# Kernel tuning notes

Measured on AMD Instinct MI355X. Metric: run time of the kernel, lower is better.

## Reference

```python
import jax, jax.numpy as jnp
import numpy as np

B, S, D = 8, 1024, 1152
H, HD = 16, 72  # num_heads, head_dim

def setup_inputs() -> dict:
    key = jax.random.key(0)
    ks = jax.random.split(key, 7)
    hidden_states = jax.random.normal(ks[0], (B, S, D), dtype=jnp.float32)
    cos = jax.random.uniform(ks[1], (S, HD), dtype=jnp.float32)
    sin = jax.random.uniform(ks[2], (S, HD), dtype=jnp.float32)
    qkv_w = jax.random.normal(ks[3], (3 * D, D), dtype=jnp.float32) * 0.02
    qkv_b = jnp.zeros((3 * D,), dtype=jnp.float32)
    proj_w = jax.random.normal(ks[4], (D, D), dtype=jnp.float32) * 0.02
    proj_b = jnp.zeros((D,), dtype=jnp.float32)
    return {"hidden_states": hidden_states, "cos": cos, "sin": sin,
            "qkv_w": qkv_w, "qkv_b": qkv_b, "proj_w": proj_w, "proj_b": proj_b}

def _rotate_half(x):
    x1, x2 = jnp.split(x, 2, axis=-1)
    return jnp.concatenate((-x2, x1), axis=-1)

def reference(hidden_states, cos, sin, qkv_w, qkv_b, proj_w, proj_b):
    b, s, d = hidden_states.shape
    # fused QKV projection
    qkv = hidden_states @ qkv_w.T + qkv_b            # [B,S,3D]
    qkv = qkv.reshape(b, s, 3, H, HD)
    qkv = jnp.transpose(qkv, (2, 0, 3, 1, 4))        # [3,B,H,S,HD]
    q, k, v = qkv[0], qkv[1], qkv[2]
    # rotary embedding, cos/sin broadcast [1,1,S,HD]
    c = cos[None, None, :, :]
    sn = sin[None, None, :, :]
    q = q * c + _rotate_half(q) * sn
    k = k * c + _rotate_half(k) * sn
    # SDPA
    scale = HD ** -0.5
    scores = jnp.einsum('bhqd,bhkd->bhqk', q, k) * scale
    probs = jax.nn.softmax(scores, axis=-1)
    attn = jnp.einsum('bhqk,bhkd->bhqd', probs, v)   # [B,H,S,HD]
    attn = jnp.transpose(attn, (0, 2, 1, 3)).reshape(b, s, d)
    return attn @ proj_w.T + proj_b
```

## Files before the change

kernel.cpp:

```cpp
#include <hip/hip_runtime.h>
#include <hip/hip_bf16.h>


typedef __attribute__((ext_vector_type(8))) short short8;
typedef __attribute__((ext_vector_type(4))) float f32x4;

__device__ __forceinline__ unsigned int f2bf(float f) {
    unsigned int u = __float_as_uint(f);
    return (u + 0x7FFFu + ((u >> 16) & 1u)) >> 16;
}
__device__ __forceinline__ float bf2f(unsigned short u) {
    return __uint_as_float((unsigned int)u << 16);
}

__device__ __forceinline__ unsigned int pk_bf16(float a, float b) {
    unsigned int r;
    asm("v_cvt_pk_bf16_f32 %0, %1, %2" : "=v"(r) : "v"(a), "v"(b));
    return r;
}

__device__ __forceinline__ void stout(float* C, size_t idx, float v) { C[idx] = v; }
__device__ __forceinline__ void stout(__hip_bfloat16* C, size_t idx, float v) {
    C[idx] = __float2bfloat16(v);
}

__device__ __forceinline__ void async_cp16(const void* g, void* l) {
    __builtin_amdgcn_global_load_lds((const __attribute__((address_space(1))) void*)g,
                                     (__attribute__((address_space(3))) void*)l, 16, 0, 0);
}

__global__ void f32_to_bf16_pair(
    const float* __restrict__ s0, unsigned short* __restrict__ d0, int n0_4,
    const float* __restrict__ s1, unsigned short* __restrict__ d1, int n1_4,
    unsigned short* __restrict__ dz, int nz_4)
{
    int i = blockIdx.x * 256 + threadIdx.x;
    if (i < n0_4) {
        float4 f = ((const float4*)s0)[i];
        ushort4 r;
        r.x = (unsigned short)f2bf(f.x);
        r.y = (unsigned short)f2bf(f.y);
        r.z = (unsigned short)f2bf(f.z);
        r.w = (unsigned short)f2bf(f.w);
        ((ushort4*)d0)[i] = r;
        return;
    }
    i -= n0_4;
    if (i < n1_4) {
        float4 f = ((const float4*)s1)[i];
        ushort4 r;
        r.x = (unsigned short)f2bf(f.x);
        r.y = (unsigned short)f2bf(f.y);
        r.z = (unsigned short)f2bf(f.z);
        r.w = (unsigned short)f2bf(f.w);
        ((ushort4*)d1)[i] = r;
        return;
    }
    i -= n1_4;
    if (i < nz_4) {
        ushort4 z; z.x = 0; z.y = 0; z.z = 0; z.w = 0;
        ((ushort4*)dz)[i] = z;
    }
}

template <int BM, int H>
__device__ __forceinline__ void stage_a(const unsigned short* __restrict__ g, int ldg,
                                        int k0, unsigned short* l, int w, int lane)
{
    if constexpr (BM == 256) {
#pragma unroll
        for (int t = 0; t < 2; t++) {
            const int c  = w * 2 + t;
            const int r0 = (c & 8) * 16 + H * 64 + (c & 7) * 8;
            const int rl = r0 + (lane >> 3);
            const int gg = (lane & 7) ^ (lane >> 3);
            async_cp16(g + (size_t)rl * ldg + k0 + gg * 8, l + r0 * 64);
        }
    } else {
        const int c  = w;
        const int r0 = (c & 4) * 16 + H * 32 + (c & 3) * 8;
        const int rl = r0 + (lane >> 3);
        const int gg = (lane & 7) ^ (lane >> 3);
        async_cp16(g + (size_t)rl * ldg + k0 + gg * 8, l + r0 * 64);
    }
}

template <int H>
__device__ __forceinline__ void stage_b(const unsigned short* __restrict__ g, int ldg,
                                        int k0, unsigned short* l, int w, int lane)
{
#pragma unroll
    for (int t = 0; t < 2; t++) {
        const int c  = w * 2 + t;
        const int r0 = (c >> 2) * 64 + H * 32 + (c & 3) * 8;
        const int rl = r0 + (lane >> 3);
        const int gg = (lane & 7) ^ (lane >> 3);
        async_cp16(g + (size_t)rl * ldg + k0 + gg * 8, l + r0 * 64);
    }
}

#define LDA(MH, SRC)                                                                   \
    _Pragma("unroll") for (int mi = 0; mi < MFRAG_; ++mi) {                            \
        Af[mi][0] = *(const short8*)((SRC) + aRow + (MH) * (BM * 16) + mi * 1024 + g0); \
        Af[mi][1] = *(const short8*)((SRC) + aRow + (MH) * (BM * 16) + mi * 1024 + g1); \
    }

#define LDB(DST, NH, SRC)                                                         \
    _Pragma("unroll") for (int ni = 0; ni < 2; ++ni) {                            \
        DST[ni][0] = *(const short8*)((SRC) + bRow + (NH) * 2048 + ni * 1024 + g0); \
        DST[ni][1] = *(const short8*)((SRC) + bRow + (NH) * 2048 + ni * 1024 + g1); \
    }

#define MFMAS(MH, NH, PB)                                                              \
    __builtin_amdgcn_s_setprio(1);                                                     \
    _Pragma("unroll") for (int mi = 0; mi < MFRAG_; ++mi)                              \
    _Pragma("unroll") for (int ni = 0; ni < 2; ++ni) {                                 \
        acc[(MH) * MFRAG_ + mi][(NH) * 2 + ni] = __builtin_amdgcn_mfma_f32_16x16x32_bf16( \
            Af[mi][0], PB[ni][0], acc[(MH) * MFRAG_ + mi][(NH) * 2 + ni], 0, 0, 0);    \
        acc[(MH) * MFRAG_ + mi][(NH) * 2 + ni] = __builtin_amdgcn_mfma_f32_16x16x32_bf16( \
            Af[mi][1], PB[ni][1], acc[(MH) * MFRAG_ + mi][(NH) * 2 + ni], 0, 0, 0);    \
    }                                                                                  \
    __builtin_amdgcn_s_setprio(0);

#define MIDBAR()                                                   \
    do {                                                           \
        __builtin_amdgcn_s_barrier();                              \
        asm volatile("s_waitcnt lgkmcnt(0)" ::: "memory");         \
        __builtin_amdgcn_sched_barrier(0);                         \
    } while (0)

#define ENDBAR()                                                   \
    do {                                                           \
        __builtin_amdgcn_s_barrier();                              \
        __builtin_amdgcn_sched_barrier(0);                         \
    } while (0)

#define GVMCNT()                                                          \
    do {                                                                  \
        if constexpr (BM == 256)                                          \
            asm volatile("s_waitcnt vmcnt(6)" ::: "memory");              \
        else                                                              \
            asm volatile("s_waitcnt vmcnt(4)" ::: "memory");              \
    } while (0)

template <typename OT, int BM>
__global__ __launch_bounds__(512, 2) void gemm_bt_256(
    const __hip_bfloat16* __restrict__ Abf,
    const __hip_bfloat16* __restrict__ Bbf,
    const float* __restrict__ bias,
    OT* __restrict__ C,
    int M, int Nreal, int K)
{
    constexpr int MFRAG_ = BM / 64;
    __shared__ __align__(16) unsigned short smem[2][(BM + 256) * 64];

    const int tid  = threadIdx.x;
    const int lane = tid & 63;
    const int w    = tid >> 6;
    const int wm   = w >> 2;
    const int wn   = w & 3;
    const int q    = lane >> 4;
    const int fr   = lane & 15;
    const int xr   = fr & 7;

    const int nwg = gridDim.x * gridDim.y;
    const int lin = blockIdx.y * gridDim.x + blockIdx.x;
    const int swz = (lin & 7) * (nwg >> 3) + (lin >> 3);
    const int bn  = (swz % gridDim.x) * 256;
    const int bm  = (swz / gridDim.x) * BM;

    const unsigned short* Ag = (const unsigned short*)Abf + (size_t)bm * K;
    const unsigned short* Bg = (const unsigned short*)Bbf + (size_t)bn * K;

    unsigned short* s00 = &smem[0][0];
    unsigned short* s01 = &smem[0][BM * 64];
    unsigned short* s10 = &smem[1][0];
    unsigned short* s11 = &smem[1][BM * 64];

    const int NT = K >> 6;
    const int NI = NT >> 1;

    const int aRow = (wm * (BM / 2) + fr) * 64;
    const int bRow = (wn * 64 + fr) * 64;
    const int g0   = ((0 * 4 + q) ^ xr) * 8;
    const int g1   = ((1 * 4 + q) ^ xr) * 8;

    f32x4 acc[2 * MFRAG_][4];
#pragma unroll
    for (int i = 0; i < 2 * MFRAG_; i++)
#pragma unroll
        for (int j = 0; j < 4; j++) acc[i][j] = (f32x4){0.f, 0.f, 0.f, 0.f};

    short8 Af[MFRAG_][2], Bf0[2][2], Bf1[2][2];

    stage_a<BM, 0>(Ag, K, 0, s00, w, lane);
    stage_a<BM, 1>(Ag, K, 0, s00, w, lane);
    stage_b<0>(Bg, K, 0, s01, w, lane);
    stage_b<1>(Bg, K, 0, s01, w, lane);
    stage_a<BM, 0>(Ag, K, 64, s10, w, lane);
    stage_b<1>(Bg, K, 64, s11, w, lane);
    stage_a<BM, 1>(Ag, K, 64, s10, w, lane);
    GVMCNT();
    ENDBAR();

#pragma unroll 1
    for (int i = 0; i < NI; i++) {
        const int k1 = (2 * i + 1) * 64;
        const int t2 = 2 * i + 2, t3 = 2 * i + 3;
        const int k2 = (t2 < NT ? t2 : NT - 1) * 64;
        const int k3 = (t3 < NT ? t3 : NT - 1) * 64;

        LDA(0, s00);
        LDB(Bf0, 0, s01);
        stage_b<0>(Bg, K, k1, s11, w, lane);
        asm volatile("s_waitcnt lgkmcnt(8)" ::: "memory");
        MIDBAR();
        MFMAS(0, 0, Bf0);
        ENDBAR();

        LDB(Bf1, 1, s01);
        stage_a<BM, 0>(Ag, K, k2, s00, w, lane);
        MIDBAR();
        MFMAS(0, 1, Bf1);
        ENDBAR();

        LDA(1, s00);
        stage_b<1>(Bg, K, k2, s01, w, lane);
        MIDBAR();
        MFMAS(1, 1, Bf1);
        ENDBAR();

        stage_a<BM, 1>(Ag, K, k2, s00, w, lane);
        GVMCNT();
        MIDBAR();
        MFMAS(1, 0, Bf0);
        ENDBAR();

        LDA(0, s10);
        LDB(Bf0, 0, s11);
        stage_b<0>(Bg, K, k2, s01, w, lane);
        asm volatile("s_waitcnt lgkmcnt(8)" ::: "memory");
        MIDBAR();
        MFMAS(0, 0, Bf0);
        ENDBAR();

        LDB(Bf1, 1, s11);
        stage_a<BM, 0>(Ag, K, k3, s10, w, lane);
        MIDBAR();
        MFMAS(0, 1, Bf1);
        ENDBAR();

        LDA(1, s10);
        stage_b<1>(Bg, K, k3, s11, w, lane);
        MIDBAR();
        MFMAS(1, 1, Bf1);
        ENDBAR();

        stage_a<BM, 1>(Ag, K, k3, s10, w, lane);
        GVMCNT();
        MIDBAR();
        MFMAS(1, 0, Bf0);
        ENDBAR();
    }

#pragma unroll
    for (int mf = 0; mf < 2 * MFRAG_; mf++) {
        const int row = bm + wm * (BM / 2) + mf * 16 + q * 4;
#pragma unroll
        for (int nf = 0; nf < 4; nf++) {
            const int col = bn + wn * 64 + nf * 16 + fr;
            if (col < Nreal) {
                const float bv = bias[col];
#pragma unroll
                for (int r = 0; r < 4; r++)
                    stout(C, (size_t)(row + r) * Nreal + col, acc[mf][nf][r] + bv);
            }
        }
    }
}

__global__ void rope_v_prep(
    const __hip_bfloat16* __restrict__ qkv,
    const float* __restrict__ cosp,
    const float* __restrict__ sinp,
    __hip_bfloat16* __restrict__ Qo,
    __hip_bfloat16* __restrict__ Ko,
    __hip_bfloat16* __restrict__ Vt)
{
    __shared__ __align__(16) unsigned short T[64 * 72];
    const int tid = threadIdx.x;
    const int bh = blockIdx.x >> 4;
    const int st = blockIdx.x & 15;
    const int b = bh >> 4, h = bh & 15;
    const size_t row0 = ((size_t)b * 1024 + st * 64) * 3456;

    const unsigned short* vsrc = (const unsigned short*)qkv + row0 + 2304 + h * 72;
#pragma unroll
    for (int k = 0; k < 3; k++) {
        const int c = tid + k * 256;
        if (c < 576) {
            const int s = c / 9, off = (c % 9) * 8;
            *(uint4*)&T[c * 8] = *(const uint4*)(vsrc + (size_t)s * 3456 + off);
        }
    }

    const unsigned short* qkvp = (const unsigned short*)qkv;
    const float QS = 0.17002324f;
#pragma unroll
    for (int k = 0; k < 3; k++) {
        const int idx = tid + k * 256;
        if (idx < 576) {
            const int sl = idx / 9, iq = idx % 9;
            const int i0 = iq * 4;
            const int sg = st * 64 + sl;
            const unsigned short* qrow = qkvp + row0 + (size_t)sl * 3456 + h * 72 + i0;

            ushort4 ql = *(const ushort4*)(qrow);
            ushort4 qh = *(const ushort4*)(qrow + 36);
            ushort4 kl = *(const ushort4*)(qrow + 1152);
            ushort4 kh = *(const ushort4*)(qrow + 1188);
            float4 cl = *(const float4*)(cosp + sg * 72 + i0);
            float4 ch = *(const float4*)(cosp + sg * 72 + i0 + 36);
            float4 nl = *(const float4*)(sinp + sg * 72 + i0);
            float4 nh = *(const float4*)(sinp + sg * 72 + i0 + 36);

            unsigned short qlv[4] = {ql.x, ql.y, ql.z, ql.w};
            unsigned short qhv[4] = {qh.x, qh.y, qh.z, qh.w};
            unsigned short klv[4] = {kl.x, kl.y, kl.z, kl.w};
            unsigned short khv[4] = {kh.x, kh.y, kh.z, kh.w};
            float clv[4] = {cl.x, cl.y, cl.z, cl.w};
            float chv[4] = {ch.x, ch.y, ch.z, ch.w};
            float nlv[4] = {nl.x, nl.y, nl.z, nl.w};
            float nhv[4] = {nh.x, nh.y, nh.z, nh.w};

            unsigned short qol[4], qoh[4], kol[4], koh[4];
#pragma unroll
            for (int j = 0; j < 4; j++) {
                const float qa = bf2f(qlv[j]), qb = bf2f(qhv[j]);
                const float ka = bf2f(klv[j]), kb = bf2f(khv[j]);
                qol[j] = (unsigned short)f2bf((qa * clv[j] - qb * nlv[j]) * QS);
                qoh[j] = (unsigned short)f2bf((qb * chv[j] + qa * nhv[j]) * QS);
                kol[j] = (unsigned short)f2bf(ka * clv[j] - kb * nlv[j]);
                koh[j] = (unsigned short)f2bf(kb * chv[j] + ka * nhv[j]);
            }
            unsigned short* qob = (unsigned short*)Qo + ((size_t)bh * 1024 + sg) * 72 + i0;
            unsigned short* kob = (unsigned short*)Ko + ((size_t)bh * 1024 + sg) * 72 + i0;
            *(ushort4*)qob        = (ushort4){qol[0], qol[1], qol[2], qol[3]};
            *(ushort4*)(qob + 36) = (ushort4){qoh[0], qoh[1], qoh[2], qoh[3]};
            *(ushort4*)kob        = (ushort4){kol[0], kol[1], kol[2], kol[3]};
            *(ushort4*)(kob + 36) = (ushort4){koh[0], koh[1], koh[2], koh[3]};
        }
    }

    __syncthreads();

    unsigned short* dst = (unsigned short*)Vt + (size_t)(bh * 16 + st) * 72 * 64;
#pragma unroll
    for (int k = 0; k < 9; k++) {
        const int o = tid + k * 256;
        const int d = o >> 5;
        const int sl = (o & 31) * 2;
        ushort2 v;
        v.x = T[sl * 72 + d];
        v.y = T[(sl + 1) * 72 + d];
        const int col = ((((sl >> 3) ^ (d & 7)) << 3)) + (sl & 7);
        *(ushort2*)&dst[d * 64 + col] = v;
    }
}

__device__ __forceinline__ void dma9(const unsigned short* g, unsigned short* l,
                                     int w, int lane)
{
#pragma unroll
    for (int c = 0; c < 3; c++) {
        const int i = w + c * 4;
        if (i < 9) async_cp16(g + i * 512 + lane * 8, l + i * 512);
    }
}

__global__ __launch_bounds__(256, 3) void attn_mfma(
    const __hip_bfloat16* __restrict__ Q,
    const __hip_bfloat16* __restrict__ K,
    const __hip_bfloat16* __restrict__ Vt,
    __hip_bfloat16* __restrict__ O)
{
    __shared__ __align__(16) unsigned short Ks[64 * 72];
    __shared__ __align__(16) unsigned short VsA[2][72 * 64];
    __shared__ __align__(16) unsigned short Vones[8 * 64];
    __shared__ __align__(16) unsigned short Ps[4][32][72];

    const int tid  = threadIdx.x;
    const int lane = tid & 63;
    const int w    = tid >> 6;
    const int quad = lane >> 4;
    const int fr   = lane & 15;
    const int bh   = blockIdx.x & 127;
    const int qt   = blockIdx.x >> 7;
    const int qbase = qt * 128 + w * 32;

    const short8 z8 = (short8){0,0,0,0,0,0,0,0};

    for (int idx = tid; idx < 512; idx += 256)
        Vones[idx] = (idx < 64) ? (unsigned short)0x3F80 : (unsigned short)0;

    const unsigned short* qp = (const unsigned short*)Q + ((size_t)bh * 1024 + qbase + fr) * 72;
    short8 qf[2][3];
#pragma unroll
    for (int sub = 0; sub < 2; sub++) {
        const unsigned short* qs = qp + sub * 16 * 72;
        qf[sub][0] = *(const short8*)(qs + quad * 8);
        qf[sub][1] = *(const short8*)(qs + 32 + quad * 8);
        qf[sub][2] = (quad == 0) ? *(const short8*)(qs + 64) : z8;
    }

    f32x4 Oa[2][5];
#pragma unroll
    for (int sub = 0; sub < 2; sub++)
#pragma unroll
        for (int n = 0; n < 5; n++) Oa[sub][n] = (f32x4){0.f, 0.f, 0.f, 0.f};

    const unsigned short* kg0 = (const unsigned short*)K + (size_t)bh * 1024 * 72;
    const unsigned short* vg0 = (const unsigned short*)Vt + (size_t)bh * 16 * 72 * 64;

    dma9(kg0, Ks, w, lane);
    dma9(vg0, &VsA[0][0], w, lane);
    dma9(vg0 + 4608, &VsA[1][0], w, lane);
    __builtin_amdgcn_sched_barrier(0);

#pragma unroll 1
    for (int t = 0; t < 16; t++) {
        if (t < 15) {
            if (w == 0) asm volatile("s_waitcnt vmcnt(3)" ::: "memory");
            else        asm volatile("s_waitcnt vmcnt(2)" ::: "memory");
        } else {
            asm volatile("s_waitcnt vmcnt(0)" ::: "memory");
        }
        __builtin_amdgcn_sched_barrier(0);
        __builtin_amdgcn_s_barrier();

        const unsigned short* vb = &VsA[t & 1][0];

#pragma unroll
        for (int nt = 0; nt < 4; nt++) {
            const unsigned short* kr = Ks + (nt * 16 + fr) * 72;
            short8 b0 = *(const short8*)(kr + quad * 8);
            short8 b1 = *(const short8*)(kr + 32 + quad * 8);
            short8 b2 = (quad == 0) ? *(const short8*)(kr + 64) : z8;
            f32x4 s0 = (f32x4){0.f, 0.f, 0.f, 0.f};
            f32x4 s1 = (f32x4){0.f, 0.f, 0.f, 0.f};
            __builtin_amdgcn_s_setprio(1);
            s0 = __builtin_amdgcn_mfma_f32_16x16x32_bf16(b0, qf[0][0], s0, 0, 0, 0);
            s1 = __builtin_amdgcn_mfma_f32_16x16x32_bf16(b0, qf[1][0], s1, 0, 0, 0);
            s0 = __builtin_amdgcn_mfma_f32_16x16x32_bf16(b1, qf[0][1], s0, 0, 0, 0);
            s1 = __builtin_amdgcn_mfma_f32_16x16x32_bf16(b1, qf[1][1], s1, 0, 0, 0);
            s0 = __builtin_amdgcn_mfma_f32_16x16x32_bf16(b2, qf[0][2], s0, 0, 0, 0);
            s1 = __builtin_amdgcn_mfma_f32_16x16x32_bf16(b2, qf[1][2], s1, 0, 0, 0);
            __builtin_amdgcn_s_setprio(0);
            uint2 p0, p1;
            p0.x = pk_bf16(__builtin_amdgcn_exp2f(s0[0]), __builtin_amdgcn_exp2f(s0[1]));
            p0.y = pk_bf16(__builtin_amdgcn_exp2f(s0[2]), __builtin_amdgcn_exp2f(s0[3]));
            p1.x = pk_bf16(__builtin_amdgcn_exp2f(s1[0]), __builtin_amdgcn_exp2f(s1[1]));
            p1.y = pk_bf16(__builtin_amdgcn_exp2f(s1[2]), __builtin_amdgcn_exp2f(s1[3]));
            *(uint2*)&Ps[w][fr][nt * 16 + quad * 4]      = p0;
            *(uint2*)&Ps[w][16 + fr][nt * 16 + quad * 4] = p1;
        }

        __builtin_amdgcn_s_barrier();
        __builtin_amdgcn_sched_barrier(0);
        if (t < 15) {
            dma9(kg0 + (size_t)(t + 1) * 4608, Ks, w, lane);
            __builtin_amdgcn_sched_barrier(0);
        }

#pragma unroll
        for (int ks = 0; ks < 2; ks++) {
            short8 ap0 = *(const short8*)&Ps[w][fr][ks * 32 + quad * 8];
            short8 ap1 = *(const short8*)&Ps[w][16 + fr][ks * 32 + quad * 8];
            const int jx8 = ((ks * 4 + quad) ^ (fr & 7)) * 8;
#pragma unroll
            for (int n = 0; n < 5; n++) {
                const unsigned short* p =
                    (n < 4) ? (vb + (n * 16 + fr) * 64 + jx8)
                            : ((fr < 8) ? (vb + (64 + fr) * 64 + jx8)
                                        : (&Vones[0] + (fr - 8) * 64 + jx8));
                short8 bv = *(const short8*)p;
                __builtin_amdgcn_s_setprio(1);
                Oa[0][n] = __builtin_amdgcn_mfma_f32_16x16x32_bf16(ap0, bv, Oa[0][n], 0, 0, 0);
                Oa[1][n] = __builtin_amdgcn_mfma_f32_16x16x32_bf16(ap1, bv, Oa[1][n], 0, 0, 0);
                __builtin_amdgcn_s_setprio(0);
            }
        }

        __builtin_amdgcn_s_barrier();
        __builtin_amdgcn_sched_barrier(0);
        if (t < 14) {
            dma9(vg0 + (size_t)(t + 2) * 4608, &VsA[t & 1][0], w, lane);
            __builtin_amdgcn_sched_barrier(0);
        }
    }

    const int lsrc = (lane & 48) | 8;
    const int b = bh >> 4, h = bh & 15;
    unsigned short* ob = (unsigned short*)O;
#pragma unroll
    for (int sub = 0; sub < 2; sub++) {
        float inv[4];
#pragma unroll
        for (int r = 0; r < 4; r++)
            inv[r] = 1.f / __shfl(Oa[sub][4][r], lsrc, 64);
#pragma unroll
        for (int n = 0; n < 5; n++) {
            const int d = n * 16 + fr;
            if (d < 72) {
#pragma unroll
                for (int r = 0; r < 4; r++) {
                    const size_t idx =
                        ((size_t)b * 1024 + qbase + sub * 16 + quad * 4 + r) * 1152 + h * 72 + d;
                    ob[idx] = (unsigned short)f2bf(Oa[sub][n][r] * inv[r]);
                }
            }
        }
    }
}

extern "C" void kernel_launch(void* const* d_in, const int* in_sizes, int n_in,
                              void* d_out, int out_size, void* d_ws, size_t ws_size,
                              hipStream_t stream)
{
    const float* hs     = (const float*)d_in[0];
    const float* cosp   = (const float*)d_in[1];
    const float* sinp   = (const float*)d_in[2];
    const float* qkv_w  = (const float*)d_in[3];
    const float* qkv_b  = (const float*)d_in[4];
    const float* proj_w = (const float*)d_in[5];
    const float* proj_b = (const float*)d_in[6];
    float* out = (float*)d_out;

    char* ws = (char*)d_ws;
    __hip_bfloat16* qkv_buf = (__hip_bfloat16*)ws;
    __hip_bfloat16* Qb = (__hip_bfloat16*)(ws + 56623104);
    __hip_bfloat16* Kb = Qb + 9437184;
    __hip_bfloat16* Vt = Kb + 9437184;
    __hip_bfloat16* Ab = qkv_buf;

    unsigned short* hs_bf = (unsigned short*)Qb;
    unsigned short* qw_bf = (unsigned short*)Kb;
    unsigned short* pw_bf = (unsigned short*)Qb;

    f32_to_bf16_pair<<<13248, 256, 0, stream>>>(hs, hs_bf, 2359296,
                                                qkv_w, qw_bf, 995328,
                                                qw_bf + 3981312, 36864);
    gemm_bt_256<__hip_bfloat16, 256>
        <<<dim3(14, 32), 512, 0, stream>>>((const __hip_bfloat16*)hs_bf,
                                           (const __hip_bfloat16*)qw_bf,
                                           qkv_b, qkv_buf, 8192, 3456, 1152);
    rope_v_prep<<<2048, 256, 0, stream>>>(qkv_buf, cosp, sinp, Qb, Kb, Vt);
    attn_mfma<<<1024, 256, 0, stream>>>(Qb, Kb, Vt, Ab);
    f32_to_bf16_pair<<<1440, 256, 0, stream>>>(proj_w, pw_bf, 331776,
                                               nullptr, nullptr, 0,
                                               pw_bf + 1327104, 36864);
    gemm_bt_256<float, 128>
        <<<dim3(5, 64), 512, 0, stream>>>((const __hip_bfloat16*)Ab,
                                          (const __hip_bfloat16*)pw_bf,
                                          proj_b, out, 8192, 1152, 1152);
}
```

Measured before the change: 303.3 us.

## Double-buffer K tiles in attention and fold proj_w conversion into first cast kernel

The attention kernel now double-buffers K alongside V, issuing one combined K+V prefetch two tiles ahead. This removes the mid-iteration barrier and K reload that used to sit between the QK and PV phases. The extra LDS lowers launch bounds from 3 to 2 blocks per CU, which risks lower occupancy. Separately, when the workspace is large enough, proj_w is converted to bf16 in the initial cast kernel into a tail region, which removes one kernel launch.

```diff
diff --git a/kernel.cpp b/kernel.cpp
--- a/kernel.cpp
+++ b/kernel.cpp
@@ -29,38 +29,52 @@
                                      (__attribute__((address_space(3))) void*)l, 16, 0, 0);
 }
 
+__device__ __forceinline__ void cvt4(const float* __restrict__ s,
+                                     unsigned short* __restrict__ d, int i)
+{
+    float4 f = ((const float4*)s)[i];
+    ushort4 r;
+    r.x = (unsigned short)f2bf(f.x);
+    r.y = (unsigned short)f2bf(f.y);
+    r.z = (unsigned short)f2bf(f.z);
+    r.w = (unsigned short)f2bf(f.w);
+    ((ushort4*)d)[i] = r;
+}
+
 __global__ void f32_to_bf16_pair(
     const float* __restrict__ s0, unsigned short* __restrict__ d0, int n0_4,
     const float* __restrict__ s1, unsigned short* __restrict__ d1, int n1_4,
     unsigned short* __restrict__ dz, int nz_4)
 {
     int i = blockIdx.x * 256 + threadIdx.x;
-    if (i < n0_4) {
-        float4 f = ((const float4*)s0)[i];
-        ushort4 r;
-        r.x = (unsigned short)f2bf(f.x);
-        r.y = (unsigned short)f2bf(f.y);
-        r.z = (unsigned short)f2bf(f.z);
-        r.w = (unsigned short)f2bf(f.w);
-        ((ushort4*)d0)[i] = r;
-        return;
-    }
+    if (i < n0_4) { cvt4(s0, d0, i); return; }
     i -= n0_4;
-    if (i < n1_4) {
-        float4 f = ((const float4*)s1)[i];
-        ushort4 r;
-        r.x = (unsigned short)f2bf(f.x);
-        r.y = (unsigned short)f2bf(f.y);
-        r.z = (unsigned short)f2bf(f.z);
-        r.w = (unsigned short)f2bf(f.w);
-        ((ushort4*)d1)[i] = r;
-        return;
-    }
+    if (i < n1_4) { cvt4(s1, d1, i); return; }
     i -= n1_4;
     if (i < nz_4) {
         ushort4 z; z.x = 0; z.y = 0; z.z = 0; z.w = 0;
         ((ushort4*)dz)[i] = z;
     }
+}
+
+__global__ void f32_to_bf16_tri(
+    const float* __restrict__ s0, unsigned short* __restrict__ d0, int n0_4,
+    const float* __restrict__ s1, unsigned short* __restrict__ d1, int n1_4,
+    unsigned short* __restrict__ dz1, int nz1_4,
+    const float* __restrict__ s2, unsigned short* __restrict__ d2, int n2_4,
+    unsigned short* __restrict__ dz2, int nz2_4)
+{
+    int i = blockIdx.x * 256 + threadIdx.x;
+    if (i < n0_4) { cvt4(s0, d0, i); return; }
+    i -= n0_4;
+    if (i < n1_4) { cvt4(s1, d1, i); return; }
+    i -= n1_4;
+    ushort4 z; z.x = 0; z.y = 0; z.z = 0; z.w = 0;
+    if (i < nz1_4) { ((ushort4*)dz1)[i] = z; return; }
+    i -= nz1_4;
+    if (i < n2_4) { cvt4(s2, d2, i); return; }
+    i -= n2_4;
+    if (i < nz2_4) ((ushort4*)dz2)[i] = z;
 }
 
 template <int BM, int H>
@@ -368,23 +382,30 @@
     }
 }
 
-__device__ __forceinline__ void dma9(const unsigned short* g, unsigned short* l,
-                                     int w, int lane)
-{
-#pragma unroll
-    for (int c = 0; c < 3; c++) {
-        const int i = w + c * 4;
-        if (i < 9) async_cp16(g + i * 512 + lane * 8, l + i * 512);
-    }
-}
-
-__global__ __launch_bounds__(256, 3) void attn_mfma(
+__device__ __forceinline__ void attn_stage(const unsigned short* kt, const unsigned short* vt,
+                                           unsigned short* kl, unsigned short* vl,
+                                           int w, int lane)
+{
+#pragma unroll
+    for (int c = 0; c < 5; c++) {
+        const int call = w + c * 4;
+        if (call < 18) {
+            const bool isv = (call >= 9);
+            const int o = (isv ? call - 9 : call) * 512;
+            const unsigned short* s = (isv ? vt : kt) + o + lane * 8;
+            unsigned short* d = (isv ? vl : kl) + o;
+            async_cp16(s, d);
+        }
+    }
+}
+
+__global__ __launch_bounds__(256, 2) void attn_mfma(
     const __hip_bfloat16* __restrict__ Q,
     const __hip_bfloat16* __restrict__ K,
     const __hip_bfloat16* __restrict__ Vt,
     __hip_bfloat16* __restrict__ O)
 {
-    __shared__ __align__(16) unsigned short Ks[64 * 72];
+    __shared__ __align__(16) unsigned short KsA[2][64 * 72];
     __shared__ __align__(16) unsigned short VsA[2][72 * 64];
     __shared__ __align__(16) unsigned short Vones[8 * 64];
     __shared__ __align__(16) unsigned short Ps[4][32][72];
@@ -422,27 +443,27 @@
     const unsigned short* kg0 = (const unsigned short*)K + (size_t)bh * 1024 * 72;
     const unsigned short* vg0 = (const unsigned short*)Vt + (size_t)bh * 16 * 72 * 64;
 
-    dma9(kg0, Ks, w, lane);
-    dma9(vg0, &VsA[0][0], w, lane);
-    dma9(vg0 + 4608, &VsA[1][0], w, lane);
+    attn_stage(kg0,        vg0,        &KsA[0][0], &VsA[0][0], w, lane);
+    attn_stage(kg0 + 4608, vg0 + 4608, &KsA[1][0], &VsA[1][0], w, lane);
     __builtin_amdgcn_sched_barrier(0);
 
 #pragma unroll 1
     for (int t = 0; t < 16; t++) {
         if (t < 15) {
-            if (w == 0) asm volatile("s_waitcnt vmcnt(3)" ::: "memory");
-            else        asm volatile("s_waitcnt vmcnt(2)" ::: "memory");
+            if (w < 2) asm volatile("s_waitcnt vmcnt(5)" ::: "memory");
+            else       asm volatile("s_waitcnt vmcnt(4)" ::: "memory");
         } else {
             asm volatile("s_waitcnt vmcnt(0)" ::: "memory");
         }
         __builtin_amdgcn_sched_barrier(0);
         __builtin_amdgcn_s_barrier();
 
-        const unsigned short* vb = &VsA[t & 1][0];
+        const unsigned short* kb = (t & 1) ? &KsA[1][0] : &KsA[0][0];
+        const unsigned short* vb = (t & 1) ? &VsA[1][0] : &VsA[0][0];
 
 #pragma unroll
         for (int nt = 0; nt < 4; nt++) {
-            const unsigned short* kr = Ks + (nt * 16 + fr) * 72;
+            const unsigned short* kr = kb + (nt * 16 + fr) * 72;
             short8 b0 = *(const short8*)(kr + quad * 8);
             short8 b1 = *(const short8*)(kr + 32 + quad * 8);
             short8 b2 = (quad == 0) ? *(const short8*)(kr + 64) : z8;
@@ -465,13 +486,6 @@
             *(uint2*)&Ps[w][16 + fr][nt * 16 + quad * 4] = p1;
         }
 
-        __builtin_amdgcn_s_barrier();
-        __builtin_amdgcn_sched_barrier(0);
-        if (t < 15) {
-            dma9(kg0 + (size_t)(t + 1) * 4608, Ks, w, lane);
-            __builtin_amdgcn_sched_barrier(0);
-        }
-
 #pragma unroll
         for (int ks = 0; ks < 2; ks++) {
             short8 ap0 = *(const short8*)&Ps[w][fr][ks * 32 + quad * 8];
@@ -493,8 +507,12 @@
 
         __builtin_amdgcn_s_barrier();
         __builtin_amdgcn_sched_barrier(0);
+
         if (t < 14) {
-            dma9(vg0 + (size_t)(t + 2) * 4608, &VsA[t & 1][0], w, lane);
+            unsigned short* kd = (t & 1) ? &KsA[1][0] : &KsA[0][0];
+            unsigned short* vd = (t & 1) ? &VsA[1][0] : &VsA[0][0];
+            attn_stage(kg0 + (size_t)(t + 2) * 4608, vg0 + (size_t)(t + 2) * 4608,
+                       kd, vd, w, lane);
             __builtin_amdgcn_sched_barrier(0);
         }
     }
@@ -545,20 +563,32 @@
 
     unsigned short* hs_bf = (unsigned short*)Qb;
     unsigned short* qw_bf = (unsigned short*)Kb;
-    unsigned short* pw_bf = (unsigned short*)Qb;
-
-    f32_to_bf16_pair<<<13248, 256, 0, stream>>>(hs, hs_bf, 2359296,
-                                                qkv_w, qw_bf, 995328,
-                                                qw_bf + 3981312, 36864);
+
+    const bool tail_ok = (ws_size >= (size_t)113246208 + 2949120);
+    unsigned short* pw_bf = tail_ok ? (unsigned short*)(ws + 113246208)
+                                    : (unsigned short*)Qb;
+
+    if (tail_ok) {
+        f32_to_bf16_tri<<<14688, 256, 0, stream>>>(
+            hs, hs_bf, 2359296,
+            qkv_w, qw_bf, 995328, qw_bf + 3981312, 36864,
+            proj_w, pw_bf, 331776, pw_bf + 1327104, 36864);
+    } else {
+        f32_to_bf16_pair<<<13248, 256, 0, stream>>>(hs, hs_bf, 2359296,
+                                                    qkv_w, qw_bf, 995328,
+                                                    qw_bf + 3981312, 36864);
+    }
     gemm_bt_256<__hip_bfloat16, 256>
         <<<dim3(14, 32), 512, 0, stream>>>((const __hip_bfloat16*)hs_bf,
                                            (const __hip_bfloat16*)qw_bf,
                                            qkv_b, qkv_buf, 8192, 3456, 1152);
     rope_v_prep<<<2048, 256, 0, stream>>>(qkv_buf, cosp, sinp, Qb, Kb, Vt);
     attn_mfma<<<1024, 256, 0, stream>>>(Qb, Kb, Vt, Ab);
-    f32_to_bf16_pair<<<1440, 256, 0, stream>>>(proj_w, pw_bf, 331776,
-                                               nullptr, nullptr, 0,
-                                               pw_bf + 1327104, 36864);
+    if (!tail_ok) {
+        f32_to_bf16_pair<<<1440, 256, 0, stream>>>(proj_w, pw_bf, 331776,
+                                                   nullptr, nullptr, 0,
+                                                   pw_bf + 1327104, 36864);
+    }
     gemm_bt_256<float, 128>
         <<<dim3(5, 64), 512, 0, stream>>>((const __hip_bfloat16*)Ab,
                                           (const __hip_bfloat16*)pw_bf,
```

Result: no change. 304.5 us (+0.4%).
